# Kernel tuning notes

Measured on AMD Instinct MI355X. Metric: run time of the kernel, lower is better.

The kernel has to match this reference:

```python
import jax, jax.numpy as jnp
import numpy as np

B, T, A, H, L = 8, 100, 64, 512, 3


def setup_inputs() -> dict:
    key = jax.random.key(0)
    ks = jax.random.split(key, 6)
    s = 1.0 / np.sqrt(H)  # PyTorch GRU init range
    x = jax.random.normal(ks[0], (B, T, A, H), jnp.float32)
    valid = jax.random.randint(ks[1], (B, T, A), 0, 2) > 0
    w_ih = jax.random.uniform(ks[2], (L, 3 * H, H), jnp.float32, -s, s)
    w_hh = jax.random.uniform(ks[3], (L, 3 * H, H), jnp.float32, -s, s)
    b_ih = jax.random.uniform(ks[4], (L, 3 * H), jnp.float32, -s, s)
    b_hh = jax.random.uniform(ks[5], (L, 3 * H), jnp.float32, -s, s)
    return {"x": x, "valid": valid, "w_ih": w_ih, "w_hh": w_hh, "b_ih": b_ih, "b_hh": b_hh}


def reference(x, valid, w_ih, w_hh, b_ih, b_hh):
    # x: [B,T,A,H], valid: [B,T,A]; multi-layer GRU over time with per-step
    # zeroing of hidden state and output where the agent is invalid.
    Bx, Tx, Ax, Hx = x.shape
    Lx = w_ih.shape[0]
    xs = jnp.transpose(x, (1, 0, 2, 3)).reshape(Tx, Bx * Ax, Hx)          # [T, BA, H]
    inv = jnp.transpose(~valid, (1, 0, 2)).reshape(Tx, Bx * Ax, 1)        # [T, BA, 1]
    h0 = jnp.zeros((Lx, Bx * Ax, Hx), x.dtype)

    def step(h, inp_t):
        xt, inv_t = inp_t                      # xt: [BA,H], inv_t: [BA,1]
        layer_in = xt
        hs = []
        for l in range(Lx):                    # small fixed layer loop
            gi = layer_in @ w_ih[l].T + b_ih[l]   # [BA, 3H]
            gh = h[l] @ w_hh[l].T + b_hh[l]       # [BA, 3H]
            i_r, i_z, i_n = jnp.split(gi, 3, axis=-1)
            h_r, h_z, h_n = jnp.split(gh, 3, axis=-1)
            r = jax.nn.sigmoid(i_r + h_r)
            z = jax.nn.sigmoid(i_z + h_z)
            n = jnp.tanh(i_n + r * h_n)
            hl = (1.0 - z) * n + z * h[l]
            hs.append(hl)
            layer_in = hl
        h_new = jnp.where(inv_t, 0.0, jnp.stack(hs))  # mask all layers' state
        y = jnp.where(inv_t, 0.0, layer_in)           # masked top-layer output
        return h_new, y

    _, ys = jax.lax.scan(step, h0, (xs, inv))         # ys: [T, BA, H]
    x1 = jnp.transpose(ys.reshape(Tx, Bx, Ax, Hx), (1, 0, 2, 3))  # [B,T,A,H]
    return x1
```

## Files before the change

kernel.cpp:

```cpp
#include <hip/hip_runtime.h>

#define Tc 100
#define Hc 512
#define Lc 3
#define H3c 1536
#define HLAY (Hc*Hc)
#define HSLOT (Lc*HLAY)
#define HLPAR (6*256*512)

typedef short bf16x8 __attribute__((ext_vector_type(8)));
typedef float f32x4 __attribute__((ext_vector_type(4)));

__device__ __forceinline__ unsigned short f2bf(float f) {
  unsigned int u = __float_as_uint(f);
  u += 0x7FFFu + ((u >> 16) & 1u);
  return (unsigned short)(u >> 16);
}

__global__ __launch_bounds__(256) void conv_bf16(const float* __restrict__ src,
                                                 unsigned short* __restrict__ dst,
                                                 int n4) {
  int i = blockIdx.x * 256 + threadIdx.x;
  if (i >= n4) return;
  f32x4 v = *(const f32x4*)(src + (size_t)i * 4);
  ushort4 o;
  o.x = f2bf(v[0]); o.y = f2bf(v[1]); o.z = f2bf(v[2]); o.w = f2bf(v[3]);
  *(ushort4*)(dst + (size_t)i * 4) = o;
}

__device__ __forceinline__ void waitg(const int* slots, int tgt, int lane) {
  const int* p = slots + (lane & 31);
  int it = 0;
  for (;;) {
    int v;
    asm volatile("global_load_dword %0, %1, off sc0 sc1\n\ts_waitcnt vmcnt(0)"
                 : "=v"(v) : "v"(p) : "memory");
    if (__all(v >= tgt)) break;
    __builtin_amdgcn_s_sleep(8);
    if (++it > 1000000) break;
  }
}

#define LOADC(dst, ptr) \
  asm volatile("global_load_dwordx4 %0, %1, off sc0 sc1" : "=v"(dst) : "v"(ptr))
#define LOADL(dst, ptr) \
  asm volatile("global_load_dwordx4 %0, %1, off sc0" : "=v"(dst) : "v"(ptr))
#define LOADN(dst, ptr) \
  asm volatile("global_load_dwordx4 %0, %1, off" : "=v"(dst) : "v"(ptr))
#define STORE_H2(ptr, v32) \
  asm volatile("global_store_short %0, %1, off sc0 sc1" :: "v"(ptr), "v"(v32))
#define STORE_HL(ptr, v32) \
  asm volatile("global_store_short %0, %1, off sc0" :: "v"(ptr), "v"(v32))
#define STORE_D(ptr, v32) \
  asm volatile("global_store_dword %0, %1, off sc0 sc1" :: "v"(ptr), "v"(v32))
#define WAITV(n) do { asm volatile("s_waitcnt vmcnt(" #n ")" ::: "memory"); \
                      __builtin_amdgcn_sched_barrier(0); } while (0)
#define MM(a, b, c) c = __builtin_amdgcn_mfma_f32_16x16x32_bf16(a, b, c, 0, 0, 0)

__global__ __launch_bounds__(1024, 4) void gru_persist16(
    const float* __restrict__ x,
    const short* __restrict__ xb,
    const short* __restrict__ wbih,
    const short* __restrict__ wbhh,
    const float* __restrict__ bih,
    const float* __restrict__ bhh,
    short* hb,
    short* hbl,
    const int* __restrict__ valid,
    float* __restrict__ y,
    int* done) {
  __shared__ char wlds[98304];

  const int bid = blockIdx.x;
  const int gi = bid & 7;
  if (gi >= 6) return;
  const int cb = bid >> 3;
  const int l = gi >> 1;
  const int rb = gi & 1;
  const int c0 = cb * 16;
  const int R0 = rb * 256;

  const int tid = threadIdx.x;
  const int w = tid >> 6;
  const int lane = tid & 63;
  const int lrow = lane & 15;
  const int kgrp = lane >> 4;

  const short* wih_l = wbih + (size_t)l * H3c * Hc;
  const short* whh_l = wbhh + (size_t)l * H3c * Hc;

#pragma unroll
  for (int it = 0; it < 6; ++it) {
    int j = it * 16 + w;
    int m = j >> 4, ks = j & 15;
    int g = (m < 3) ? m : m - 3;
    int n = g * Hc + c0 + lrow;
    const short* src = ((m < 3) ? wih_l : whh_l) + (size_t)n * Hc + ks * 32 + kgrp * 8;
    *(bf16x8*)(wlds + (size_t)j * 1024 + lane * 16) = *(const bf16x8*)src;
  }
  __syncthreads();

  const char* wl = wlds + (lane << 4);

  const float* bihl = bih + l * H3c;
  const float* bhhl = bhh + l * H3c;
  const int c = c0 + lrow;
  const float bi0 = bihl[c], bi1 = bihl[Hc + c], bi2 = bihl[2 * Hc + c];
  const float bh0 = bhhl[c], bh1 = bhhl[Hc + c], bh2 = bhhl[2 * Hc + c];

  f32x4 hreg = f32x4{0.f, 0.f, 0.f, 0.f};

  WAITV(0);

  for (int t = 0; t < Tc; ++t) {
    if (w == 1 && t > 0)           waitg(done + gi * 32, t, lane);
    if (w == 2 && l < 2 && t >= 3) waitg(done + ((l + 1) * 2 + rb) * 32, t - 2, lane);
    __syncthreads();

    const int par = t & 1;
    const int s3 = t % 3;
    const int rowl = w * 16 + lrow;

    const short* pHL = hbl + (size_t)(1 - par) * HLPAR + (size_t)gi * 131072
                       + (size_t)rowl * Hc;
    const short* pA = nullptr;
    const float* pXf = x;
    {
      int row = R0 + rowl;
      if (l > 0) {
        pA = hb + (size_t)s3 * HSLOT + (size_t)(l - 1) * HLAY + (size_t)row * Hc;
      } else {
        int bb = row >> 6, aa = row & 63;
        size_t rofs = ((size_t)bb * Tc + t) * 64 + aa;
        if (xb) pA = xb + rofs * Hc;
        pXf = x + rofs * Hc;
      }
    }

    f32x4 acc[6];
#pragma unroll
    for (int m = 0; m < 6; ++m) acc[m] = f32x4{0.f, 0.f, 0.f, 0.f};

#define ISS4(LOADM, P_, R_, b)                                                     \
      { _Pragma("unroll") for (int q = 0; q < 4; ++q) {                            \
          const int ks = (b) + q;                                                  \
          LOADM(R_[ks & 7], P_ + ks * 32 + (kgrp << 3));                           \
        } }
#define CON4(R_, b, M0)                                                            \
      { _Pragma("unroll") for (int q = 0; q < 4; ++q) {                            \
          const int ks = (b) + q;                                                  \
          bf16x8 B0 = *(const bf16x8*)(wl + (((M0) * 16 + ks) << 10));             \
          bf16x8 B1 = *(const bf16x8*)(wl + ((((M0) + 1) * 16 + ks) << 10));       \
          bf16x8 B2 = *(const bf16x8*)(wl + ((((M0) + 2) * 16 + ks) << 10));       \
          MM(R_[ks & 7], B0, acc[(M0)]);                                           \
          MM(R_[ks & 7], B1, acc[(M0) + 1]);                                       \
          MM(R_[ks & 7], B2, acc[(M0) + 2]);                                       \
        } }
#define PASS(LOADM, P_, M0)                                                        \
      { bf16x8 R_[8];                                                              \
        ISS4(LOADM, P_, R_, 0);  ISS4(LOADM, P_, R_, 4);                           \
        WAITV(4); CON4(R_, 0, M0);                                                 \
        ISS4(LOADM, P_, R_, 8);                                                    \
        WAITV(4); CON4(R_, 4, M0);                                                 \
        ISS4(LOADM, P_, R_, 12);                                                   \
        WAITV(4); CON4(R_, 8, M0);                                                 \
        WAITV(0); CON4(R_, 12, M0);                                                \
      }

    __builtin_amdgcn_sched_barrier(0);
    if (t > 0) {
      PASS(LOADL, pHL, 3)
    }
    if (l > 0) {
      if (w == 0) waitg(done + ((l - 1) * 2 + rb) * 32, t + 1, lane);
      __syncthreads();
      __builtin_amdgcn_sched_barrier(0);
      PASS(LOADC, pA, 0)
    } else if (xb) {
      PASS(LOADN, pA, 0)
    } else {
#pragma unroll
      for (int ks = 0; ks < 16; ++ks) {
        const float* _px = pXf + ks * 32 + (kgrp << 3);
        f32x4 v0 = *(const f32x4*)_px;
        f32x4 v1 = *(const f32x4*)(_px + 4);
        bf16x8 t_;
#pragma unroll
        for (int e = 0; e < 4; ++e) {
          t_[e] = (short)f2bf(v0[e]); t_[4 + e] = (short)f2bf(v1[e]);
        }
        bf16x8 B0 = *(const bf16x8*)(wl + ((0 * 16 + ks) << 10));
        bf16x8 B1 = *(const bf16x8*)(wl + ((1 * 16 + ks) << 10));
        bf16x8 B2 = *(const bf16x8*)(wl + ((2 * 16 + ks) << 10));
        MM(t_, B0, acc[0]);
        MM(t_, B1, acc[1]);
        MM(t_, B2, acc[2]);
      }
    }
    __builtin_amdgcn_sched_barrier(0);

    short* hout = hb + (size_t)s3 * HSLOT + (size_t)l * HLAY;
    short* houtL = hbl + (size_t)par * HLPAR + (size_t)gi * 131072;
#pragma unroll
    for (int rr = 0; rr < 4; ++rr) {
      int mloc = w * 16 + kgrp * 4 + rr;
      int rowg = R0 + mloc;
      int bb = rowg >> 6, aa = rowg & 63;
      size_t vofs = ((size_t)bb * Tc + t) * 64 + aa;
      int vld = valid[vofs];
      float ir = acc[0][rr] + bi0;
      float iz = acc[1][rr] + bi1;
      float in_ = acc[2][rr] + bi2;
      float hr = acc[3][rr] + bh0;
      float hz = acc[4][rr] + bh1;
      float hn = acc[5][rr] + bh2;
      float rg = 1.0f / (1.0f + __expf(-(ir + hr)));
      float zg = 1.0f / (1.0f + __expf(-(iz + hz)));
      float ng = tanhf(in_ + rg * hn);
      float hnew = (1.0f - zg) * ng + zg * hreg[rr];
      if (!vld) hnew = 0.0f;
      hreg[rr] = hnew;
      int hv = (int)f2bf(hnew);
      STORE_HL(houtL + (size_t)mloc * Hc + c, hv);
      if (l < 2) STORE_H2(hout + (size_t)rowg * Hc + c, hv);
      else       y[vofs * Hc + c] = hnew;
    }

    asm volatile("s_waitcnt vmcnt(0)" ::: "memory");
    __syncthreads();
    if (tid == 0) {
      int v = t + 1;
      STORE_D(done + gi * 32 + cb, v);
    }
    WAITV(0);
  }
}

extern "C" void kernel_launch(void* const* d_in, const int* in_sizes, int n_in,
                              void* d_out, int out_size, void* d_ws, size_t ws_size,
                              hipStream_t stream) {
  const float* x = (const float*)d_in[0];
  const int* valid = (const int*)d_in[1];
  const float* w_ih = (const float*)d_in[2];
  const float* w_hh = (const float*)d_in[3];
  const float* b_ih = (const float*)d_in[4];
  const float* b_hh = (const float*)d_in[5];
  float* y = (float*)d_out;

  char* ws = (char*)d_ws;
  const size_t welems = (size_t)Lc * H3c * Hc;
  unsigned short* wbih = (unsigned short*)ws;
  unsigned short* wbhh = (unsigned short*)(ws + welems * 2);
  short* hb = (short*)(ws + welems * 4);
  const size_t hb_bytes = (size_t)3 * HSLOT * 2;
  int* done = (int*)(ws + welems * 4 + hb_bytes);
  const size_t flags_bytes = 4800;
  const size_t hbl_off = welems * 4 + hb_bytes + flags_bytes;
  const size_t hbl_bytes = (size_t)2 * HLPAR * 2;
  short* hbl = (short*)(ws + hbl_off);
  const size_t xb_off = hbl_off + hbl_bytes;
  const size_t xelems = (size_t)8 * Tc * 64 * Hc;
  const bool big = ws_size >= xb_off + xelems * 2;
  unsigned short* xbf = big ? (unsigned short*)(ws + xb_off) : nullptr;

  int n4w = (int)(welems / 4);
  conv_bf16<<<(n4w + 255) / 256, 256, 0, stream>>>(w_ih, wbih, n4w);
  conv_bf16<<<(n4w + 255) / 256, 256, 0, stream>>>(w_hh, wbhh, n4w);
  if (big) {
    int n4x = (int)(xelems / 4);
    conv_bf16<<<(n4x + 255) / 256, 256, 0, stream>>>(x, xbf, n4x);
  }
  (void)hipMemsetAsync(hb, 0, hb_bytes + flags_bytes, stream);

  gru_persist16<<<256, 1024, 0, stream>>>(x, (const short*)xbf,
                                          (const short*)wbih, (const short*)wbhh,
                                          b_ih, b_hh, hb, hbl, valid, y, done);
}
```

Measured before the change: 2.060 ms.

## Merge hidden and input gate GEMM passes behind a single upfront dependency wait

Moves the wait on the lower layer's completion flag to the top of each timestep, before the shared barrier, which removes a second block-wide barrier in the middle of the step. The recurrent-hidden and layer-input matmul passes are fused into one interleaved pass that issues both sets of global loads together and runs six MFMA chains per k-slice. This gives more loads in flight and less serialization. In exchange, the recurrent matmul can no longer start before the previous layer's output is ready, and register pressure rises from doubling the load buffers.

```diff
diff --git a/kernel.cpp b/kernel.cpp
--- a/kernel.cpp
+++ b/kernel.cpp
@@ -57,7 +57,7 @@
                       __builtin_amdgcn_sched_barrier(0); } while (0)
 #define MM(a, b, c) c = __builtin_amdgcn_mfma_f32_16x16x32_bf16(a, b, c, 0, 0, 0)
 
-__global__ __launch_bounds__(1024, 4) void gru_persist16(
+__global__ __launch_bounds__(1024, 4) void gru_persist18(
     const float* __restrict__ x,
     const short* __restrict__ xb,
     const short* __restrict__ wbih,
@@ -113,6 +113,7 @@
   WAITV(0);
 
   for (int t = 0; t < Tc; ++t) {
+    if (w == 0 && l > 0)           waitg(done + ((l - 1) * 2 + rb) * 32, t + 1, lane);
     if (w == 1 && t > 0)           waitg(done + gi * 32, t, lane);
     if (w == 2 && l < 2 && t >= 3) waitg(done + ((l + 1) * 2 + rb) * 32, t - 2, lane);
     __syncthreads();
@@ -141,6 +142,38 @@
 #pragma unroll
     for (int m = 0; m < 6; ++m) acc[m] = f32x4{0.f, 0.f, 0.f, 0.f};
 
+#define ISSM(ALOAD, b)                                                             \
+      { _Pragma("unroll") for (int q = 0; q < 4; ++q) {                            \
+          const int ks = (b) + q;                                                  \
+          LOADL(RH[ks & 7], pHL + ks * 32 + (kgrp << 3));                          \
+          ALOAD(RA[ks & 7], pA + ks * 32 + (kgrp << 3));                           \
+        } }
+#define CONM(b)                                                                    \
+      { _Pragma("unroll") for (int q = 0; q < 4; ++q) {                            \
+          const int ks = (b) + q;                                                  \
+          bf16x8 B0 = *(const bf16x8*)(wl + ((0 * 16 + ks) << 10));                \
+          bf16x8 B1 = *(const bf16x8*)(wl + ((1 * 16 + ks) << 10));                \
+          bf16x8 B2 = *(const bf16x8*)(wl + ((2 * 16 + ks) << 10));                \
+          bf16x8 B3 = *(const bf16x8*)(wl + ((3 * 16 + ks) << 10));                \
+          bf16x8 B4 = *(const bf16x8*)(wl + ((4 * 16 + ks) << 10));                \
+          bf16x8 B5 = *(const bf16x8*)(wl + ((5 * 16 + ks) << 10));                \
+          MM(RA[ks & 7], B0, acc[0]);                                              \
+          MM(RA[ks & 7], B1, acc[1]);                                              \
+          MM(RA[ks & 7], B2, acc[2]);                                              \
+          MM(RH[ks & 7], B3, acc[3]);                                              \
+          MM(RH[ks & 7], B4, acc[4]);                                              \
+          MM(RH[ks & 7], B5, acc[5]);                                              \
+        } }
+#define MERGED(ALOAD)                                                              \
+      { bf16x8 RH[8], RA[8];                                                       \
+        ISSM(ALOAD, 0);  ISSM(ALOAD, 4);                                           \
+        WAITV(8); CONM(0);                                                         \
+        ISSM(ALOAD, 8);                                                            \
+        WAITV(8); CONM(4);                                                         \
+        ISSM(ALOAD, 12);                                                           \
+        WAITV(8); CONM(8);                                                         \
+        WAITV(0); CONM(12);                                                        \
+      }
 #define ISS4(LOADM, P_, R_, b)                                                     \
       { _Pragma("unroll") for (int q = 0; q < 4; ++q) {                            \
           const int ks = (b) + q;                                                  \
@@ -168,17 +201,12 @@
       }
 
     __builtin_amdgcn_sched_barrier(0);
-    if (t > 0) {
-      PASS(LOADL, pHL, 3)
-    }
     if (l > 0) {
-      if (w == 0) waitg(done + ((l - 1) * 2 + rb) * 32, t + 1, lane);
-      __syncthreads();
-      __builtin_amdgcn_sched_barrier(0);
-      PASS(LOADC, pA, 0)
+      if (t > 0) { MERGED(LOADC) } else { PASS(LOADC, pA, 0) }
     } else if (xb) {
-      PASS(LOADN, pA, 0)
+      if (t > 0) { MERGED(LOADN) } else { PASS(LOADN, pA, 0) }
     } else {
+      if (t > 0) { PASS(LOADL, pHL, 3) }
 #pragma unroll
       for (int ks = 0; ks < 16; ++ks) {
         const float* _px = pXf + ks * 32 + (kgrp << 3);
@@ -272,7 +300,7 @@
   }
   (void)hipMemsetAsync(hb, 0, hb_bytes + flags_bytes, stream);
 
-  gru_persist16<<<256, 1024, 0, stream>>>(x, (const short*)xbf,
+  gru_persist18<<<256, 1024, 0, stream>>>(x, (const short*)xbf,
                                           (const short*)wbih, (const short*)wbhh,
                                           b_ih, b_hh, hb, hbl, valid, y, done);
 }
```

Measured after the change: 2.695 ms. +30.9%, slower.
